# Kernel optimization log

Measured on AMD Instinct MI355X. Metric: run time of the kernel, lower is better.

Reference implementation:

```python
import jax, jax.numpy as jnp
import numpy as np

N = 100000      # nodes
E = 1600000     # edges (avg degree 16)
IN, HID, OUT = 128, 128, 64


def setup_inputs() -> dict:
    key = jax.random.key(0)
    k1, k2, k3, k4 = jax.random.split(key, 4)
    x = jax.random.normal(k1, (N, IN), dtype=jnp.float32)
    edge_index = jax.random.randint(k2, (2, E), 0, N, dtype=jnp.int64)
    # GCNConv linear weights (glorot-ish scale) and zero biases
    W1 = jax.random.normal(k3, (IN, HID), dtype=jnp.float32) * (1.0 / np.sqrt(IN))
    b1 = jnp.zeros((HID,), jnp.float32)
    W2 = jax.random.normal(k4, (HID, OUT), dtype=jnp.float32) * (1.0 / np.sqrt(HID))
    b2 = jnp.zeros((OUT,), jnp.float32)
    return {"x": x, "edge_index": edge_index, "W1": W1, "b1": b1, "W2": W2, "b2": b2}


def reference(x, edge_index, W1, b1, W2, b2):
    n = x.shape[0]
    loops = jnp.arange(n, dtype=edge_index.dtype)
    self_e = jnp.stack([loops, loops])  # [2, N]
    # forward() explicitly adds self-loops, then PyG GCNConv's gcn_norm
    # (add_self_loops=True by default) adds a second set -> duplicate (i,i) edges.
    ei = jnp.concatenate([edge_index, self_e, self_e], axis=1)
    row, col = ei[0], ei[1]  # source, target

    # symmetric normalization: deg over target index, norm_e = d^-1/2[row]*d^-1/2[col]
    deg = jax.ops.segment_sum(jnp.ones(row.shape, x.dtype), col, num_segments=n)
    dis = jax.lax.rsqrt(deg)  # deg >= 2 thanks to self-loops
    norm = dis[row] * dis[col]  # [E']

    def gcn_conv(h, W, b):
        h = h @ W                               # transform first (PyG order)
        msg = h[row] * norm[:, None]            # gather + per-edge scale
        agg = jax.ops.segment_sum(msg, col, num_segments=n)  # scatter-add
        return agg + b

    h = jax.nn.relu(gcn_conv(x, W1, b1))
    return gcn_conv(h, W2, b2)
```

## Files before the change

### kernel.cpp

```cpp
#include <hip/hip_runtime.h>
#include <hip/hip_fp16.h>

#define NPB   512
#define NBMAX 256
#define CHUNK 2048

using f16x4 = __attribute__((ext_vector_type(4))) _Float16;
using f32x4 = __attribute__((ext_vector_type(4))) float;

__global__ void k_detect(const int* __restrict__ ei32, int* __restrict__ flag,
                         int* __restrict__ bcur, int nb, int cap) {
  int t = threadIdx.x;
  if (t < nb) bcur[t] = t * cap;
  if (t == 0) {
    int z = 1;
    for (int k = 0; k < 64; ++k)
      if (ei32[2 * k + 1] != 0) { z = 0; break; }
    flag[0] = z;
  }
}

__device__ __forceinline__ int edge_at(const void* ei, int is64, long long pos) {
  return is64 ? (int)((const long long*)ei)[pos] : ((const int*)ei)[pos];
}

__device__ void fillB_body(char* smem, const void* __restrict__ ei,
                           const int* __restrict__ flag, int E,
                           int* __restrict__ bcur, int* __restrict__ tmp,
                           int nb, int bid, int nblk) {
  int* cntL   = (int*)smem;
  int* startL = cntL + NBMAX;
  int* curL   = startL + NBMAX;
  int* gofs   = curL + NBMAX;
  int* sh     = gofs + NBMAX;
  int* stage  = sh + NBMAX;
  unsigned char* sbkt = (unsigned char*)(stage + CHUNK);
  int t = threadIdx.x;
  int is64 = flag[0];
  for (long long base = (long long)bid * CHUNK; base < E;
       base += (long long)nblk * CHUNK) {
    int m = (int)min((long long)CHUNK, (long long)E - base);
    cntL[t] = 0;
    __syncthreads();
    for (int i = t; i < m; i += 256) {
      int c = edge_at(ei, is64, (long long)E + base + i);
      atomicAdd(&cntL[c >> 9], 1);
    }
    __syncthreads();
    sh[t] = cntL[t];
    __syncthreads();
    for (int off = 1; off < NBMAX; off <<= 1) {
      int x = 0;
      if (t >= off) x = sh[t - off];
      __syncthreads();
      if (t >= off) sh[t] += x;
      __syncthreads();
    }
    int excl = t ? sh[t - 1] : 0;
    startL[t] = excl;
    curL[t] = excl;
    if (t < nb && cntL[t] > 0) gofs[t] = atomicAdd(&bcur[t], cntL[t]);
    __syncthreads();
    for (int i = t; i < m; i += 256) {
      int r = edge_at(ei, is64, base + i);
      int c = edge_at(ei, is64, (long long)E + base + i);
      int b = c >> 9;
      int p = atomicAdd(&curL[b], 1);
      stage[p] = ((c & 511) << 17) | r;
      sbkt[p] = (unsigned char)b;
    }
    __syncthreads();
    for (int i = t; i < m; i += 256) {
      int b = sbkt[i];
      tmp[gofs[b] + (i - startL[b])] = stage[i];
    }
    __syncthreads();
  }
}

template <int BN, bool AHALF, bool PRESCALE>
__device__ void gemm_body(char* smem, const void* __restrict__ Av,
                          const float* __restrict__ W,
                          const float* __restrict__ dis,
                          __half* __restrict__ C, int M, int tiles,
                          int bid, int nblk) {
  _Float16 (*Wt)[136] = (_Float16(*)[136])smem;
  _Float16 (*At)[136] = (_Float16(*)[136])(smem + sizeof(_Float16) * BN * 136);
  float* disL = (float*)(smem + sizeof(_Float16) * (BN + 64) * 136);
  constexpr int NT = BN / 64;
  constexpr int CH = BN / 4;
  int t = threadIdx.x;
  int lane = t & 63, w = t >> 6;
  int lrow = lane & 15;
  int kq = (lane >> 4) * 4;
  int wcol0 = w * (BN / 4);

  for (int idx = t; idx < 128 * BN / 4; idx += 256) {
    int k = idx / CH, c4 = (idx % CH) * 4;
    float4 v = *(const float4*)&W[(size_t)k * BN + c4];
    Wt[c4 + 0][k] = (_Float16)v.x;
    Wt[c4 + 1][k] = (_Float16)v.y;
    Wt[c4 + 2][k] = (_Float16)v.z;
    Wt[c4 + 3][k] = (_Float16)v.w;
  }

  for (int tile = bid; tile < tiles; tile += nblk) {
    int row0 = tile * 64;
    __syncthreads();
#pragma unroll
    for (int i = 0; i < 8; ++i) {
      int idx = t + i * 256;
      int r = idx >> 5, c = (idx & 31) * 4;
      int gr = row0 + r;
      f16x4 hv = {0, 0, 0, 0};
      if (gr < M) {
        if constexpr (AHALF) {
          hv = *(const f16x4*)&((const _Float16*)Av)[(size_t)gr * 128 + c];
        } else {
          float4 v = *(const float4*)&((const float*)Av)[(size_t)gr * 128 + c];
          hv = f16x4{(_Float16)v.x, (_Float16)v.y, (_Float16)v.z, (_Float16)v.w};
        }
      }
      *(f16x4*)&At[r][c] = hv;
    }
    if constexpr (PRESCALE) {
      if (t < 64) {
        int gr = row0 + t;
        disL[t] = (gr < M) ? dis[gr] : 0.f;
      }
    }
    __syncthreads();
    f32x4 acc[4][NT];
#pragma unroll
    for (int mt = 0; mt < 4; ++mt)
#pragma unroll
      for (int nt = 0; nt < NT; ++nt) acc[mt][nt] = f32x4{0.f, 0.f, 0.f, 0.f};
#pragma unroll
    for (int k0 = 0; k0 < 128; k0 += 16) {
      int kk = k0 + kq;
      f16x4 a[4], b[NT];
#pragma unroll
      for (int mt = 0; mt < 4; ++mt)
        a[mt] = *(const f16x4*)&At[mt * 16 + lrow][kk];
#pragma unroll
      for (int nt = 0; nt < NT; ++nt)
        b[nt] = *(const f16x4*)&Wt[wcol0 + nt * 16 + lrow][kk];
#pragma unroll
      for (int mt = 0; mt < 4; ++mt)
#pragma unroll
        for (int nt = 0; nt < NT; ++nt)
          acc[mt][nt] = __builtin_amdgcn_mfma_f32_16x16x16f16(a[mt], b[nt],
                                                              acc[mt][nt], 0, 0, 0);
    }
    __syncthreads();
#pragma unroll
    for (int mt = 0; mt < 4; ++mt)
#pragma unroll
      for (int nt = 0; nt < NT; ++nt) {
        int cc = wcol0 + nt * 16 + lrow;
        int rr = mt * 16 + kq;
#pragma unroll
        for (int reg = 0; reg < 4; ++reg) {
          float val = acc[mt][nt][reg];
          if constexpr (PRESCALE) val *= disL[rr + reg];
          At[rr + reg][cc] = (_Float16)val;
        }
      }
    __syncthreads();
#pragma unroll
    for (int i = 0; i < BN / 16; ++i) {
      int idx = t + i * 256;
      int r = idx / CH, c = (idx % CH) * 4;
      int gr = row0 + r;
      if (gr < M)
        *(f16x4*)&C[(size_t)gr * BN + c] = *(const f16x4*)&At[r][c];
    }
  }
}

__global__ __launch_bounds__(256) void k_mega1(
    const void* __restrict__ x, const float* __restrict__ W1,
    __half* __restrict__ t1, int M, int tiles,
    const void* __restrict__ ei, const int* __restrict__ flag, int E,
    int* __restrict__ bcur, int* __restrict__ tmp, int nb) {
  extern __shared__ char smem[];
  if (blockIdx.x & 1)
    fillB_body(smem, ei, flag, E, bcur, tmp, nb, blockIdx.x >> 1, gridDim.x >> 1);
  else
    gemm_body<128, false, false>(smem, x, W1, nullptr, t1, M, tiles,
                                 blockIdx.x >> 1, gridDim.x >> 1);
}

__global__ __launch_bounds__(256) void k_gemm2(
    const void* __restrict__ Av, const float* __restrict__ W,
    const float* __restrict__ dis, __half* __restrict__ C, int M, int tiles) {
  extern __shared__ char smem[];
  gemm_body<64, true, true>(smem, Av, W, dis, C, M, tiles, blockIdx.x, gridDim.x);
}

__global__ void k_bscan(const int* __restrict__ bcur, int cap,
                        int* __restrict__ bbase, int* __restrict__ rowptr,
                        int nb, int N, int E) {
  __shared__ int sh[NBMAX];
  int t = threadIdx.x;
  sh[t] = (t < nb) ? (bcur[t] - t * cap) : 0;
  __syncthreads();
  for (int off = 1; off < NBMAX; off <<= 1) {
    int x = 0;
    if (t >= off) x = sh[t - off];
    __syncthreads();
    if (t >= off) sh[t] += x;
    __syncthreads();
  }
  int excl = t ? sh[t - 1] : 0;
  if (t < nb) bbase[t] = excl;
  if (t == 0) { bbase[nb] = E; rowptr[N] = E; }
}

__global__ __launch_bounds__(256) void k_fillC(const int* __restrict__ tmp,
                                               const int* __restrict__ bcur,
                                               const int* __restrict__ bbase,
                                               int cap, int* __restrict__ rowptr,
                                               float* __restrict__ dis,
                                               int* __restrict__ esrc,
                                               __half* __restrict__ t1, int N) {
  __shared__ int cnt[NPB];
  __shared__ int loc[NPB];
  __shared__ float disS[NPB];
  __shared__ int sh[256];
  int b = blockIdx.x, t = threadIdx.x;
  int beg = b * cap;
  int end = bcur[b];
  int outb = bbase[b];
  int base_node = b << 9;
  cnt[t] = 0; cnt[t + 256] = 0;
  __syncthreads();
  for (int e = beg + t; e < end; e += 256)
    atomicAdd(&cnt[tmp[e] >> 17], 1);
  __syncthreads();
  int c0 = cnt[2 * t], c1 = cnt[2 * t + 1];
  sh[t] = c0 + c1;
  __syncthreads();
  for (int off = 1; off < 256; off <<= 1) {
    int x = 0;
    if (t >= off) x = sh[t - off];
    __syncthreads();
    if (t >= off) sh[t] += x;
    __syncthreads();
  }
  int pre = t ? sh[t - 1] : 0;
  loc[2 * t] = outb + pre;
  loc[2 * t + 1] = outb + pre + c0;
  float d0 = rsqrtf((float)(c0 + 2)), d1 = rsqrtf((float)(c1 + 2));
  disS[2 * t] = d0; disS[2 * t + 1] = d1;
  int v0 = base_node + 2 * t, v1 = v0 + 1;
  if (v0 < N) { rowptr[v0] = outb + pre;      dis[v0] = d0; }
  if (v1 < N) { rowptr[v1] = outb + pre + c0; dis[v1] = d1; }
  __syncthreads();
  for (int e = beg + t; e < end; e += 256) {
    int u = tmp[e];
    int pos = atomicAdd(&loc[u >> 17], 1);
    esrc[pos] = u & 0x1FFFF;
  }
  for (int idx = t; idx < NPB * 16; idx += 256) {
    int row = idx >> 4, ch = (idx & 15) * 8;
    int v = base_node + row;
    if (v < N) {
      size_t ofs = (size_t)v * 128 + ch;
      uint4 u = *(const uint4*)&t1[ofs];
      float dsc = disS[row];
      __half2* hp = (__half2*)&u;
#pragma unroll
      for (int j = 0; j < 4; ++j) {
        float lo = __low2float(hp[j]) * dsc, hi = __high2float(hp[j]) * dsc;
        hp[j] = __floats2half2_rn(lo, hi);
      }
      *(uint4*)&t1[ofs] = u;
    }
  }
}

#define ACC4(u)                                                         \
  { __half2 p;                                                          \
    p = *(__half2*)&(u).x; a0 += __low2float(p); a1 += __high2float(p); \
    p = *(__half2*)&(u).y; a2 += __low2float(p); a3 += __high2float(p); }

__global__ __launch_bounds__(256) void k_gather128(const __half* __restrict__ t,
    const float* __restrict__ bias, const int* __restrict__ rowptr,
    const int* __restrict__ esrc, const float* __restrict__ dis,
    __half* __restrict__ o, int n) {
  int gw = (int)((blockIdx.x * blockDim.x + threadIdx.x) >> 6);
  int lane = threadIdx.x & 63;
  int nw = (int)((gridDim.x * blockDim.x) >> 6);
  int half = lane >> 5;
  int f = (lane & 31) * 4;
  for (int v = gw; v < n; v += nw) {
    float a0 = 0.f, a1 = 0.f, a2 = 0.f, a3 = 0.f;
    int beg = rowptr[v], end = rowptr[v + 1];
    int e = beg + half;
    for (; e + 14 < end; e += 16) {
      int s0 = esrc[e],      s1 = esrc[e + 2],  s2 = esrc[e + 4],  s3 = esrc[e + 6];
      int s4 = esrc[e + 8],  s5 = esrc[e + 10], s6 = esrc[e + 12], s7 = esrc[e + 14];
      uint2 u0 = *(const uint2*)&t[(size_t)s0 * 128 + f];
      uint2 u1 = *(const uint2*)&t[(size_t)s1 * 128 + f];
      uint2 u2 = *(const uint2*)&t[(size_t)s2 * 128 + f];
      uint2 u3 = *(const uint2*)&t[(size_t)s3 * 128 + f];
      uint2 u4 = *(const uint2*)&t[(size_t)s4 * 128 + f];
      uint2 u5 = *(const uint2*)&t[(size_t)s5 * 128 + f];
      uint2 u6 = *(const uint2*)&t[(size_t)s6 * 128 + f];
      uint2 u7 = *(const uint2*)&t[(size_t)s7 * 128 + f];
      ACC4(u0) ACC4(u1) ACC4(u2) ACC4(u3)
      ACC4(u4) ACC4(u5) ACC4(u6) ACC4(u7)
    }
    for (; e + 6 < end; e += 8) {
      int s0 = esrc[e], s1 = esrc[e + 2], s2 = esrc[e + 4], s3 = esrc[e + 6];
      uint2 u0 = *(const uint2*)&t[(size_t)s0 * 128 + f];
      uint2 u1 = *(const uint2*)&t[(size_t)s1 * 128 + f];
      uint2 u2 = *(const uint2*)&t[(size_t)s2 * 128 + f];
      uint2 u3 = *(const uint2*)&t[(size_t)s3 * 128 + f];
      ACC4(u0) ACC4(u1) ACC4(u2) ACC4(u3)
    }
    for (; e < end; e += 2) {
      int s0 = esrc[e];
      uint2 u0 = *(const uint2*)&t[(size_t)s0 * 128 + f];
      ACC4(u0)
    }
    if (half == 0) {
      uint2 uv = *(const uint2*)&t[(size_t)v * 128 + f];
      __half2 p;
      p = *(__half2*)&uv.x; a0 = fmaf(2.f, __low2float(p), a0); a1 = fmaf(2.f, __high2float(p), a1);
      p = *(__half2*)&uv.y; a2 = fmaf(2.f, __low2float(p), a2); a3 = fmaf(2.f, __high2float(p), a3);
    }
    a0 += __shfl_xor(a0, 32); a1 += __shfl_xor(a1, 32);
    a2 += __shfl_xor(a2, 32); a3 += __shfl_xor(a3, 32);
    if (half == 0) {
      float dv = dis[v];
      a0 = fmaxf(fmaf(dv, a0, bias[f]),     0.f);
      a1 = fmaxf(fmaf(dv, a1, bias[f + 1]), 0.f);
      a2 = fmaxf(fmaf(dv, a2, bias[f + 2]), 0.f);
      a3 = fmaxf(fmaf(dv, a3, bias[f + 3]), 0.f);
      __half2 h0 = __floats2half2_rn(a0, a1), h1 = __floats2half2_rn(a2, a3);
      uint2 uu;
      uu.x = *(unsigned int*)&h0; uu.y = *(unsigned int*)&h1;
      *(uint2*)&o[(size_t)v * 128 + f] = uu;
    }
  }
}

__global__ __launch_bounds__(256) void k_gather64(const __half* __restrict__ t,
    const float* __restrict__ bias, const int* __restrict__ rowptr,
    const int* __restrict__ esrc, const float* __restrict__ dis,
    float* __restrict__ o, int n) {
  int gw = (int)((blockIdx.x * blockDim.x + threadIdx.x) >> 6);
  int lane = threadIdx.x & 63;
  int nw = (int)((gridDim.x * blockDim.x) >> 6);
  int sub = lane >> 4;
  int f = (lane & 15) * 4;
  for (int v = gw; v < n; v += nw) {
    float a0 = 0.f, a1 = 0.f, a2 = 0.f, a3 = 0.f;
    int beg = rowptr[v], end = rowptr[v + 1];
    int e = beg + sub;
    for (; e + 12 < end; e += 16) {
      int s0 = esrc[e], s1 = esrc[e + 4], s2 = esrc[e + 8], s3 = esrc[e + 12];
      uint2 u0 = *(const uint2*)&t[(size_t)s0 * 64 + f];
      uint2 u1 = *(const uint2*)&t[(size_t)s1 * 64 + f];
      uint2 u2 = *(const uint2*)&t[(size_t)s2 * 64 + f];
      uint2 u3 = *(const uint2*)&t[(size_t)s3 * 64 + f];
      ACC4(u0) ACC4(u1) ACC4(u2) ACC4(u3)
    }
    for (; e < end; e += 4) {
      int s0 = esrc[e];
      uint2 u0 = *(const uint2*)&t[(size_t)s0 * 64 + f];
      ACC4(u0)
    }
    if (sub == 0) {
      uint2 uv = *(const uint2*)&t[(size_t)v * 64 + f];
      __half2 p;
      p = *(__half2*)&uv.x; a0 = fmaf(2.f, __low2float(p), a0); a1 = fmaf(2.f, __high2float(p), a1);
      p = *(__half2*)&uv.y; a2 = fmaf(2.f, __low2float(p), a2); a3 = fmaf(2.f, __high2float(p), a3);
    }
    a0 += __shfl_xor(a0, 16); a0 += __shfl_xor(a0, 32);
    a1 += __shfl_xor(a1, 16); a1 += __shfl_xor(a1, 32);
    a2 += __shfl_xor(a2, 16); a2 += __shfl_xor(a2, 32);
    a3 += __shfl_xor(a3, 16); a3 += __shfl_xor(a3, 32);
    if (sub == 0) {
      float dv = dis[v];
      float4 r;
      r.x = fmaf(dv, a0, bias[f]);     r.y = fmaf(dv, a1, bias[f + 1]);
      r.z = fmaf(dv, a2, bias[f + 2]); r.w = fmaf(dv, a3, bias[f + 3]);
      *(float4*)&o[(size_t)v * 64 + f] = r;
    }
  }
}

extern "C" void kernel_launch(void* const* d_in, const int* in_sizes, int n_in,
                              void* d_out, int out_size, void* d_ws, size_t ws_size,
                              hipStream_t stream) {
  const float* x  = (const float*)d_in[0];
  const void*  ei = d_in[1];
  const float* W1 = (const float*)d_in[2];
  const float* b1 = (const float*)d_in[3];
  const float* W2 = (const float*)d_in[4];
  const float* b2 = (const float*)d_in[5];
  const int N = in_sizes[0] / 128;
  const int E = in_sizes[1] / 2;
  float* out = (float*)d_out;
  const int nb  = (N + NPB - 1) / NPB;
  const int cap = E / nb + 4096;

  size_t off = 0;
  auto alloc = [&](size_t bytes) -> void* {
    void* p = (char*)d_ws + off;
    off += (bytes + 255) & ~(size_t)255;
    return p;
  };
  int*    flag   = (int*)alloc(4);
  int*    bcur   = (int*)alloc(NBMAX * 4);
  int*    bbase  = (int*)alloc((NBMAX + 1) * 4);
  int*    rowptr = (int*)alloc(((size_t)N + 1) * 4);
  float*  dis    = (float*)alloc((size_t)N * 4);
  int*    tmp    = (int*)alloc(((size_t)nb * cap + 16384) * 4);
  int*    esrc   = (int*)alloc((size_t)E * 4);
  __half* t1     = (__half*)alloc((size_t)N * 128 * 2);
  __half* z1     = (__half*)alloc((size_t)N * 128 * 2);
  __half* t2     = t1;

  int tiles = (N + 63) / 64;
  const int smem_mega  = (128 + 64) * 136 * 2 + 256;
  const int smem_gemm2 = (64 + 64) * 136 * 2 + 256;

  k_detect<<<1, 256, 0, stream>>>((const int*)ei, flag, bcur, nb, cap);
  k_mega1<<<1550, 256, smem_mega, stream>>>(x, W1, t1, N, tiles,
                                            ei, flag, E, bcur, tmp, nb);
  k_bscan<<<1, 256, 0, stream>>>(bcur, cap, bbase, rowptr, nb, N, E);
  k_fillC<<<nb, 256, 0, stream>>>(tmp, bcur, bbase, cap, rowptr, dis, esrc, t1, N);

  k_gather128<<<2048, 256, 0, stream>>>(t1, b1, rowptr, esrc, dis, z1, N);
  k_gemm2<<<min(tiles, 768), 256, smem_gemm2, stream>>>(z1, W2, dis, t2, N, tiles);
  k_gather64<<<2048, 256, 0, stream>>>(t2, b2, rowptr, esrc, dis, out, N);
}
```

Measured before the change: 228.4 us.

## Split fused GEMM1/edge-bucketing megakernel into separate GEMM and fill kernels

Splits the combined kernel, whose blocks alternated between the first dense GEMM and edge bucketing, into two launches. The GEMM runs with 768 persistent blocks, and the bucketing kernel uses one block per 2048-edge chunk with static shared memory. This removes the shared-memory footprint coupling and the grid-stride bucketing loop, letting the bucketing blocks run at higher occupancy with their own smaller shared allocation. In exchange the two stages no longer overlap on the GPU and an extra launch is added.

```diff
diff --git a/kernel.cpp b/kernel.cpp
--- a/kernel.cpp
+++ b/kernel.cpp
@@ -24,57 +24,52 @@
   return is64 ? (int)((const long long*)ei)[pos] : ((const int*)ei)[pos];
 }
 
-__device__ void fillB_body(char* smem, const void* __restrict__ ei,
-                           const int* __restrict__ flag, int E,
-                           int* __restrict__ bcur, int* __restrict__ tmp,
-                           int nb, int bid, int nblk) {
-  int* cntL   = (int*)smem;
-  int* startL = cntL + NBMAX;
-  int* curL   = startL + NBMAX;
-  int* gofs   = curL + NBMAX;
-  int* sh     = gofs + NBMAX;
-  int* stage  = sh + NBMAX;
-  unsigned char* sbkt = (unsigned char*)(stage + CHUNK);
+__global__ __launch_bounds__(256) void k_fillB(const void* __restrict__ ei,
+                                               const int* __restrict__ flag, int E,
+                                               int* __restrict__ bcur,
+                                               int* __restrict__ tmp, int nb) {
+  __shared__ int cntL[NBMAX], startL[NBMAX], curL[NBMAX], gofs[NBMAX];
+  __shared__ int sh[NBMAX];
+  __shared__ int stage[CHUNK];
+  __shared__ unsigned char sbkt[CHUNK];
   int t = threadIdx.x;
   int is64 = flag[0];
-  for (long long base = (long long)bid * CHUNK; base < E;
-       base += (long long)nblk * CHUNK) {
-    int m = (int)min((long long)CHUNK, (long long)E - base);
-    cntL[t] = 0;
-    __syncthreads();
-    for (int i = t; i < m; i += 256) {
-      int c = edge_at(ei, is64, (long long)E + base + i);
-      atomicAdd(&cntL[c >> 9], 1);
-    }
-    __syncthreads();
-    sh[t] = cntL[t];
-    __syncthreads();
-    for (int off = 1; off < NBMAX; off <<= 1) {
-      int x = 0;
-      if (t >= off) x = sh[t - off];
-      __syncthreads();
-      if (t >= off) sh[t] += x;
-      __syncthreads();
-    }
-    int excl = t ? sh[t - 1] : 0;
-    startL[t] = excl;
-    curL[t] = excl;
-    if (t < nb && cntL[t] > 0) gofs[t] = atomicAdd(&bcur[t], cntL[t]);
-    __syncthreads();
-    for (int i = t; i < m; i += 256) {
-      int r = edge_at(ei, is64, base + i);
-      int c = edge_at(ei, is64, (long long)E + base + i);
-      int b = c >> 9;
-      int p = atomicAdd(&curL[b], 1);
-      stage[p] = ((c & 511) << 17) | r;
-      sbkt[p] = (unsigned char)b;
-    }
-    __syncthreads();
-    for (int i = t; i < m; i += 256) {
-      int b = sbkt[i];
-      tmp[gofs[b] + (i - startL[b])] = stage[i];
-    }
-    __syncthreads();
+  long long base = (long long)blockIdx.x * CHUNK;
+  if (base >= E) return;
+  int m = (int)min((long long)CHUNK, (long long)E - base);
+  cntL[t] = 0;
+  __syncthreads();
+  for (int i = t; i < m; i += 256) {
+    int c = edge_at(ei, is64, (long long)E + base + i);
+    atomicAdd(&cntL[c >> 9], 1);
+  }
+  __syncthreads();
+  sh[t] = cntL[t];
+  __syncthreads();
+  for (int off = 1; off < NBMAX; off <<= 1) {
+    int x = 0;
+    if (t >= off) x = sh[t - off];
+    __syncthreads();
+    if (t >= off) sh[t] += x;
+    __syncthreads();
+  }
+  int excl = t ? sh[t - 1] : 0;
+  startL[t] = excl;
+  curL[t] = excl;
+  if (t < nb && cntL[t] > 0) gofs[t] = atomicAdd(&bcur[t], cntL[t]);
+  __syncthreads();
+  for (int i = t; i < m; i += 256) {
+    int r = edge_at(ei, is64, base + i);
+    int c = edge_at(ei, is64, (long long)E + base + i);
+    int b = c >> 9;
+    int p = atomicAdd(&curL[b], 1);
+    stage[p] = ((c & 511) << 17) | r;
+    sbkt[p] = (unsigned char)b;
+  }
+  __syncthreads();
+  for (int i = t; i < m; i += 256) {
+    int b = sbkt[i];
+    tmp[gofs[b] + (i - startL[b])] = stage[i];
   }
 }
 
@@ -178,17 +173,12 @@
   }
 }
 
-__global__ __launch_bounds__(256) void k_mega1(
+__global__ __launch_bounds__(256) void k_gemm1(
     const void* __restrict__ x, const float* __restrict__ W1,
-    __half* __restrict__ t1, int M, int tiles,
-    const void* __restrict__ ei, const int* __restrict__ flag, int E,
-    int* __restrict__ bcur, int* __restrict__ tmp, int nb) {
+    __half* __restrict__ t1, int M, int tiles) {
   extern __shared__ char smem[];
-  if (blockIdx.x & 1)
-    fillB_body(smem, ei, flag, E, bcur, tmp, nb, blockIdx.x >> 1, gridDim.x >> 1);
-  else
-    gemm_body<128, false, false>(smem, x, W1, nullptr, t1, M, tiles,
-                                 blockIdx.x >> 1, gridDim.x >> 1);
+  gemm_body<128, false, false>(smem, x, W1, nullptr, t1, M, tiles,
+                               blockIdx.x, gridDim.x);
 }
 
 __global__ __launch_bounds__(256) void k_gemm2(
@@ -426,12 +416,13 @@
   __half* t2     = t1;
 
   int tiles = (N + 63) / 64;
-  const int smem_mega  = (128 + 64) * 136 * 2 + 256;
+  int nchunks = (E + CHUNK - 1) / CHUNK;
+  const int smem_gemm1 = (128 + 64) * 136 * 2 + 256;
   const int smem_gemm2 = (64 + 64) * 136 * 2 + 256;
 
   k_detect<<<1, 256, 0, stream>>>((const int*)ei, flag, bcur, nb, cap);
-  k_mega1<<<1550, 256, smem_mega, stream>>>(x, W1, t1, N, tiles,
-                                            ei, flag, E, bcur, tmp, nb);
+  k_gemm1<<<768, 256, smem_gemm1, stream>>>(x, W1, t1, N, tiles);
+  k_fillB<<<nchunks, 256, 0, stream>>>(ei, flag, E, bcur, tmp, nb);
   k_bscan<<<1, 256, 0, stream>>>(bcur, cap, bbase, rowptr, nb, N, E);
   k_fillC<<<nb, 256, 0, stream>>>(tmp, bcur, bbase, cap, rowptr, dis, esrc, t1, N);
 
```

Result: no change. 230.7 us (+1.0%).
